# Kernel tuning notes

Measured on AMD Instinct MI355X. Metric: run time of the kernel, lower is better.

Reference implementation:

```python
import jax, jax.numpy as jnp
import numpy as np

B, T, E, H = 4, 1024, 1024, 16
D = E // H  # head_dim = 64


def setup_inputs() -> dict:
    key = jax.random.key(0)
    ks = jax.random.split(key, 6)
    s = 0.02  # realistic init scale for stable softmax
    return {
        "hidden_states": jax.random.normal(ks[0], (B, T, E), jnp.float32),
        "attention_mask": jnp.zeros((B, 1, T, T), jnp.float32),
        "Wq": jax.random.normal(ks[1], (E, E), jnp.float32) * s,
        "bq": jnp.zeros((E,), jnp.float32),
        "Wk": jax.random.normal(ks[2], (E, E), jnp.float32) * s,
        "bk": jnp.zeros((E,), jnp.float32),
        "Wv": jax.random.normal(ks[3], (E, E), jnp.float32) * s,
        "bv": jnp.zeros((E,), jnp.float32),
        "Wo": jax.random.normal(ks[4], (E, E), jnp.float32) * s,
        "bo": jnp.zeros((E,), jnp.float32),
    }


def reference(hidden_states, attention_mask, Wq, bq, Wk, bk, Wv, bv, Wo, bo):
    b, t, e = hidden_states.shape
    scaling = jnp.asarray(D, hidden_states.dtype) ** -0.5
    # q_proj weights/bias are pre-scaled in the module; equivalent to scaling q output
    q = (hidden_states @ Wq.T + bq) * scaling      # [B,T,E]
    k = hidden_states @ Wk.T + bk                   # self-attention path (no cache)
    v = hidden_states @ Wv.T + bv
    q = q.reshape(b, t, H, D)
    k = k.reshape(b, t, H, D)
    v = v.reshape(b, t, H, D)
    # bmm(q, k^T): [B,H,T,S] score matrix (materialized, as in the original)
    scores = jnp.einsum("bthd,bshd->bhts", q, k) + attention_mask
    probs = jax.nn.softmax(scores, axis=-1)
    ctx = jnp.einsum("bhts,bshd->bthd", probs, v).reshape(b, t, e)
    return ctx @ Wo.T + bo
```

## Files before the change

kernel.cpp:

```cpp
#include <hip/hip_runtime.h>
#include <math.h>

#define BB 4
#define TT 1024
#define EE 1024
#define HH 16
#define DD 64
#define KDIM 1024
#define N_HS (4096 * 1024)
#define N_W  (1024 * 1024)
#define NQKV (BB * HH * TT * DD)

typedef _Float16 f16x8 __attribute__((ext_vector_type(8)));
typedef float    f32x4 __attribute__((ext_vector_type(4)));

__device__ __forceinline__ unsigned short f2h(float x) {
    _Float16 h = (_Float16)x;
    return __builtin_bit_cast(unsigned short, h);
}
__device__ __forceinline__ void split_h(float x, unsigned short& hi, unsigned short& lo) {
    _Float16 h = (_Float16)x;
    hi = __builtin_bit_cast(unsigned short, h);
    lo = f2h(x - (float)h);
}

__device__ __forceinline__ void gload16(const void* g, void* l) {
    __builtin_amdgcn_global_load_lds(
        (const __attribute__((address_space(1))) void*)g,
        (__attribute__((address_space(3))) void*)l, 16, 0, 0);
}

__global__ __launch_bounds__(256)
void split_kernel(const float* __restrict__ hs,
                  const float* __restrict__ Wq, const float* __restrict__ Wk,
                  const float* __restrict__ Wv, const float* __restrict__ Wo,
                  unsigned short* __restrict__ ws)
{
    const int u = blockIdx.x * 256 + threadIdx.x;
    const float* src;
    unsigned short* dst;
    if (u < (N_HS / 4)) {
        src = hs + (size_t)u * 4;
        dst = ws + (size_t)u * 4;
    } else {
        int v = u - N_HS / 4;
        int wsel = v >> 18;
        int wo   = v & 0x3FFFF;
        const float* Wsrc = (wsel == 0) ? Wq : (wsel == 1) ? Wk : (wsel == 2) ? Wv : Wo;
        src = Wsrc + (size_t)wo * 4;
        dst = ws + (size_t)N_HS + (size_t)wsel * N_W + (size_t)wo * 4;
    }
    float4 x = *(const float4*)src;
    ushort4 h4;
    h4.x = f2h(x.x); h4.y = f2h(x.y); h4.z = f2h(x.z); h4.w = f2h(x.w);
    *(ushort4*)dst = h4;
}

__global__ __launch_bounds__(256)
void qkv_kernel(const unsigned short* __restrict__ hsp,
                const unsigned short* __restrict__ wqp,
                const float* __restrict__ bq, const float* __restrict__ bk,
                const float* __restrict__ bv,
                unsigned short* __restrict__ qkvb)
{
    __shared__ unsigned short Ah[128 * 32], Bh[128 * 32];

    const int widx  = blockIdx.x >> 3;
    const int nbase = (blockIdx.x & 7) * 128;
    const int mbase = blockIdx.y * 128;
    const unsigned short* Wp = wqp + (size_t)widx * N_W;
    const float* bias = (widx == 0) ? bq : (widx == 1) ? bk : bv;
    unsigned short* dst = qkvb + (size_t)widx * NQKV;
    const float scale = (widx == 0) ? 0.125f : 1.0f;

    const int tid  = threadIdx.x;
    const int w    = tid >> 6;
    const int lane = tid & 63;
    const int quad = lane >> 4;
    const int l16  = lane & 15;
    const int wm   = (w >> 1) * 64;
    const int wn   = (w & 1) * 64;

    f32x4 acc[4][4];
#pragma unroll
    for (int i = 0; i < 4; i++)
#pragma unroll
        for (int j = 0; j < 4; j++) acc[i][j] = (f32x4)0.f;

#pragma unroll 1
    for (int kt = 0; kt < KDIM; kt += 32) {
        __syncthreads();
#pragma unroll
        for (int i = 0; i < 2; i++) {
            int u = tid + i * 256;
            int r = u >> 2, c = u & 3;
            int q = c ^ ((r >> 1) & 3);
            gload16(hsp + (size_t)(mbase + r) * KDIM + kt + q * 8, &Ah[u * 8]);
            gload16(Wp  + (size_t)(nbase + r) * KDIM + kt + q * 8, &Bh[u * 8]);
        }
        __syncthreads();

        f16x8 af[4], bfr[4];
#pragma unroll
        for (int i = 0; i < 4; i++) {
            int r = wm + i * 16 + l16;
            af[i] = *(const f16x8*)&Ah[(r * 4 + (quad ^ ((r >> 1) & 3))) * 8];
        }
#pragma unroll
        for (int j = 0; j < 4; j++) {
            int r = wn + j * 16 + l16;
            bfr[j] = *(const f16x8*)&Bh[(r * 4 + (quad ^ ((r >> 1) & 3))) * 8];
        }
#pragma unroll
        for (int i = 0; i < 4; i++)
#pragma unroll
            for (int j = 0; j < 4; j++)
                acc[i][j] = __builtin_amdgcn_mfma_f32_16x16x32_f16(af[i], bfr[j], acc[i][j], 0, 0, 0);
    }

#pragma unroll
    for (int j = 0; j < 4; j++) {
        int n = nbase + wn + j * 16 + l16;
        int h = n >> 6, d = n & 63;
        float bj = bias[n];
#pragma unroll
        for (int i = 0; i < 4; i++)
#pragma unroll
            for (int rr = 0; rr < 4; rr++) {
                int m = mbase + wm + i * 16 + quad * 4 + rr;
                int b = m >> 10, t = m & 1023;
                dst[(((size_t)(b * HH + h) * TT + t) * DD + d)] =
                    f2h((acc[i][j][rr] + bj) * scale);
            }
    }
}

__global__ __launch_bounds__(256)
void outproj_kernel(const unsigned short* __restrict__ ctxh,
                    const unsigned short* __restrict__ ctxl,
                    const unsigned short* __restrict__ wop,
                    const float* __restrict__ bo, float* __restrict__ out)
{
    __shared__ unsigned short Ach[64 * 32], Acl[64 * 32], Bh[128 * 32];

    const int nbase = blockIdx.x * 128;
    const int mbase = blockIdx.y * 64;

    const int tid  = threadIdx.x;
    const int w    = tid >> 6;
    const int lane = tid & 63;
    const int quad = lane >> 4;
    const int l16  = lane & 15;
    const int wm   = (w >> 1) * 32;
    const int wn   = (w & 1) * 64;

    f32x4 acc[2][4];
#pragma unroll
    for (int i = 0; i < 2; i++)
#pragma unroll
        for (int j = 0; j < 4; j++) acc[i][j] = (f32x4)0.f;

#pragma unroll 1
    for (int kt = 0; kt < KDIM; kt += 32) {
        __syncthreads();
        {
            int r = tid >> 2, c = tid & 3;
            int q = c ^ ((r >> 1) & 3);
            size_t ga = (size_t)(mbase + r) * KDIM + kt + q * 8;
            gload16(ctxh + ga, &Ach[tid * 8]);
            gload16(ctxl + ga, &Acl[tid * 8]);
        }
#pragma unroll
        for (int i = 0; i < 2; i++) {
            int u = tid + i * 256;
            int r = u >> 2, c = u & 3;
            int q = c ^ ((r >> 1) & 3);
            gload16(wop + (size_t)(nbase + r) * KDIM + kt + q * 8, &Bh[u * 8]);
        }
        __syncthreads();

        f16x8 ah[2], al[2], bfr[4];
#pragma unroll
        for (int i = 0; i < 2; i++) {
            int r = wm + i * 16 + l16;
            int slot = (r * 4 + (quad ^ ((r >> 1) & 3))) * 8;
            ah[i] = *(const f16x8*)&Ach[slot];
            al[i] = *(const f16x8*)&Acl[slot];
        }
#pragma unroll
        for (int j = 0; j < 4; j++) {
            int r = wn + j * 16 + l16;
            bfr[j] = *(const f16x8*)&Bh[(r * 4 + (quad ^ ((r >> 1) & 3))) * 8];
        }
#pragma unroll
        for (int i = 0; i < 2; i++)
#pragma unroll
            for (int j = 0; j < 4; j++) {
                acc[i][j] = __builtin_amdgcn_mfma_f32_16x16x32_f16(ah[i], bfr[j], acc[i][j], 0, 0, 0);
                acc[i][j] = __builtin_amdgcn_mfma_f32_16x16x32_f16(al[i], bfr[j], acc[i][j], 0, 0, 0);
            }
    }

#pragma unroll
    for (int j = 0; j < 4; j++) {
        int n = nbase + wn + j * 16 + l16;
        float bj = bo[n];
#pragma unroll
        for (int i = 0; i < 2; i++)
#pragma unroll
            for (int rr = 0; rr < 4; rr++) {
                int m = mbase + wm + i * 16 + quad * 4 + rr;
                out[(size_t)m * EE + n] = acc[i][j][rr] + bj;
            }
    }
}

#define LS 72

__global__ __launch_bounds__(256)
void attn_kernel(const unsigned short* __restrict__ qp_, const unsigned short* __restrict__ kp_,
                 const unsigned short* __restrict__ vp_,
                 const float* __restrict__ mask,
                 unsigned short* __restrict__ ctxh, unsigned short* __restrict__ ctxl)
{
    __shared__ unsigned short Ks[64 * 64];
    __shared__ unsigned short Vt[64 * LS];
    __shared__ unsigned short Ps[64 * LS];

    const int bh = blockIdx.y;
    const int b  = bh >> 4;
    const int h  = bh & 15;
    const int m0 = blockIdx.x * 64;
    const size_t hoff = (size_t)bh * TT * DD;
    const unsigned short* qhp = qp_ + hoff;
    const unsigned short* khp = kp_ + hoff;
    const unsigned short* vhp = vp_ + hoff;
    const float* mb = mask + (size_t)b * TT * TT;

    const int tid  = threadIdx.x;
    const int w    = tid >> 6;
    const int lane = tid & 63;
    const int quad = lane >> 4;
    const int l16  = lane & 15;

    f16x8 qf[2];
#pragma unroll
    for (int s = 0; s < 2; s++)
        qf[s] = *(const f16x8*)(qhp + (size_t)(m0 + w * 16 + l16) * DD + s * 32 + quad * 8);

    f32x4 o[4];
    float m_i[4], l_i[4];
#pragma unroll
    for (int t = 0; t < 4; t++) o[t] = (f32x4)0.f;
#pragma unroll
    for (int r = 0; r < 4; r++) { m_i[r] = -INFINITY; l_i[r] = 0.f; }

    for (int n0 = 0; n0 < TT; n0 += 64) {
        float mreg[4][4];
#pragma unroll
        for (int t = 0; t < 4; t++)
#pragma unroll
            for (int r = 0; r < 4; r++)
                mreg[t][r] = mb[(size_t)(m0 + w * 16 + quad * 4 + r) * TT + n0 + 16 * t + l16];

        __syncthreads();
#pragma unroll
        for (int i = 0; i < 2; i++) {
            int u = tid + i * 256;
            int r = u >> 3, cp = u & 7;
            int c = cp ^ (r & 7);
            gload16(khp + (size_t)(n0 + r) * DD + c * 8, &Ks[u * 8]);
        }
        {
            int n  = tid & 63;
            int d0 = (tid >> 6) * 8;
#pragma unroll
            for (int half = 0; half < 2; half++) {
                int dd = d0 + half * 32;
                uint4 rv = *(const uint4*)(vhp + (size_t)(n0 + n) * DD + dd);
                unsigned int uu[4] = {rv.x, rv.y, rv.z, rv.w};
#pragma unroll
                for (int j = 0; j < 4; j++) {
                    Vt[(dd + 2 * j + 0) * LS + n] = (unsigned short)(uu[j] & 0xFFFFu);
                    Vt[(dd + 2 * j + 1) * LS + n] = (unsigned short)(uu[j] >> 16);
                }
            }
        }
        __syncthreads();

        f32x4 st[4];
#pragma unroll
        for (int t = 0; t < 4; t++) {
            f32x4 sv;
            sv[0] = mreg[t][0]; sv[1] = mreg[t][1]; sv[2] = mreg[t][2]; sv[3] = mreg[t][3];
            st[t] = sv;
        }
#pragma unroll
        for (int s = 0; s < 2; s++)
#pragma unroll
            for (int t = 0; t < 4; t++) {
                int R = 16 * t + l16;
                const f16x8 kf = *(const f16x8*)&Ks[(R * 8 + ((s * 4 + quad) ^ (R & 7))) * 8];
                st[t] = __builtin_amdgcn_mfma_f32_16x16x32_f16(qf[s], kf, st[t], 0, 0, 0);
            }

        float rm[4], rs[4], alpha[4];
#pragma unroll
        for (int r = 0; r < 4; r++)
            rm[r] = fmaxf(fmaxf(st[0][r], st[1][r]), fmaxf(st[2][r], st[3][r]));
#pragma unroll
        for (int mky = 1; mky < 16; mky <<= 1)
#pragma unroll
            for (int r = 0; r < 4; r++)
                rm[r] = fmaxf(rm[r], __shfl_xor(rm[r], mky));
#pragma unroll
        for (int r = 0; r < 4; r++) {
            float mn = fmaxf(m_i[r], rm[r]);
            alpha[r] = __expf(m_i[r] - mn);
            m_i[r]   = mn;
            rs[r]    = 0.f;
        }
#pragma unroll
        for (int t = 0; t < 4; t++)
#pragma unroll
            for (int r = 0; r < 4; r++) {
                float p = __expf(st[t][r] - m_i[r]);
                st[t][r] = p;
                rs[r] += p;
            }
#pragma unroll
        for (int mky = 1; mky < 16; mky <<= 1)
#pragma unroll
            for (int r = 0; r < 4; r++)
                rs[r] += __shfl_xor(rs[r], mky);
#pragma unroll
        for (int r = 0; r < 4; r++)
            l_i[r] = l_i[r] * alpha[r] + rs[r];
#pragma unroll
        for (int t = 0; t < 4; t++)
#pragma unroll
            for (int r = 0; r < 4; r++)
                o[t][r] *= alpha[r];

#pragma unroll
        for (int t = 0; t < 4; t++)
#pragma unroll
            for (int r = 0; r < 4; r++)
                Ps[(w * 16 + quad * 4 + r) * LS + 16 * t + l16] = f2h(st[t][r]);

#pragma unroll
        for (int s = 0; s < 2; s++) {
            const f16x8 pf = *(const f16x8*)&Ps[(w * 16 + l16) * LS + s * 32 + quad * 8];
#pragma unroll
            for (int t = 0; t < 4; t++) {
                const f16x8 vf = *(const f16x8*)&Vt[(16 * t + l16) * LS + s * 32 + quad * 8];
                o[t] = __builtin_amdgcn_mfma_f32_16x16x32_f16(pf, vf, o[t], 0, 0, 0);
            }
        }
    }

#pragma unroll
    for (int r = 0; r < 4; r++) {
        float inv = 1.0f / l_i[r];
        int m = m0 + w * 16 + quad * 4 + r;
#pragma unroll
        for (int t = 0; t < 4; t++) {
            float val = o[t][r] * inv;
            unsigned short hi, lo;
            split_h(val, hi, lo);
            size_t off = (size_t)(b * TT + m) * EE + h * DD + 16 * t + l16;
            ctxh[off] = hi;
            ctxl[off] = lo;
        }
    }
}

extern "C" void kernel_launch(void* const* d_in, const int* in_sizes, int n_in,
                              void* d_out, int out_size, void* d_ws, size_t ws_size,
                              hipStream_t stream)
{
    const float* hs   = (const float*)d_in[0];
    const float* mask = (const float*)d_in[1];
    const float* Wq   = (const float*)d_in[2];
    const float* bq   = (const float*)d_in[3];
    const float* Wk   = (const float*)d_in[4];
    const float* bk   = (const float*)d_in[5];
    const float* Wv   = (const float*)d_in[6];
    const float* bv   = (const float*)d_in[7];
    const float* Wo   = (const float*)d_in[8];
    const float* bo   = (const float*)d_in[9];
    float* out = (float*)d_out;

    unsigned short* ws   = (unsigned short*)d_ws;
    unsigned short* hsp  = ws;
    unsigned short* wqp  = ws + (size_t)N_HS;
    unsigned short* wop  = wqp + 3 * (size_t)N_W;
    unsigned short* qkvb = wqp + 4 * (size_t)N_W;
    unsigned short* qp   = qkvb;
    unsigned short* kp   = qp + (size_t)NQKV;
    unsigned short* vp   = kp + (size_t)NQKV;
    unsigned short* ctxh = ws;
    unsigned short* ctxl = qkvb + 3 * (size_t)NQKV;

    split_kernel<<<8192, 256, 0, stream>>>(hs, Wq, Wk, Wv, Wo, ws);
    qkv_kernel<<<dim3(24, 32), 256, 0, stream>>>(hsp, wqp, bq, bk, bv, qkvb);
    attn_kernel<<<dim3(TT / 64, BB * HH), 256, 0, stream>>>(qp, kp, vp, mask, ctxh, ctxl);
    outproj_kernel<<<dim3(8, 64), 256, 0, stream>>>(ctxh, ctxl, wop, bo, out);
}
```

Measured before the change: 230.6 us.

## Pre-transpose V in a separate kernel and async-load it into swizzled LDS

```diff
diff --git a/kernel.cpp b/kernel.cpp
--- a/kernel.cpp
+++ b/kernel.cpp
@@ -136,6 +136,40 @@
 }
 
 __global__ __launch_bounds__(256)
+void vtrans_kernel(const unsigned short* __restrict__ vp,
+                   unsigned short* __restrict__ vtp)
+{
+    __shared__ unsigned short Ts[64 * 72];
+    const int bh = blockIdx.y;
+    const int t0 = blockIdx.x * 64;
+    const unsigned short* src = vp  + (size_t)bh * TT * DD + (size_t)t0 * DD;
+    unsigned short*       dst = vtp + (size_t)bh * DD * TT + t0;
+    const int tid = threadIdx.x;
+
+#pragma unroll
+    for (int i = 0; i < 2; i++) {
+        int id = tid + i * 256;
+        int r = id >> 3, c = id & 7;
+        *(uint4*)&Ts[r * 72 + c * 8] = *(const uint4*)(src + (size_t)r * DD + c * 8);
+    }
+    __syncthreads();
+#pragma unroll
+    for (int i = 0; i < 2; i++) {
+        int id = tid + i * 256;
+        int d = id >> 3, c = id & 7;
+        unsigned short tmp[8];
+#pragma unroll
+        for (int j = 0; j < 8; j++) tmp[j] = Ts[(c * 8 + j) * 72 + d];
+        uint4 o;
+        o.x = (unsigned int)tmp[0] | ((unsigned int)tmp[1] << 16);
+        o.y = (unsigned int)tmp[2] | ((unsigned int)tmp[3] << 16);
+        o.z = (unsigned int)tmp[4] | ((unsigned int)tmp[5] << 16);
+        o.w = (unsigned int)tmp[6] | ((unsigned int)tmp[7] << 16);
+        *(uint4*)(dst + (size_t)d * TT + c * 8) = o;
+    }
+}
+
+__global__ __launch_bounds__(256)
 void outproj_kernel(const unsigned short* __restrict__ ctxh,
                     const unsigned short* __restrict__ ctxl,
                     const unsigned short* __restrict__ wop,
@@ -219,12 +253,12 @@
 
 __global__ __launch_bounds__(256)
 void attn_kernel(const unsigned short* __restrict__ qp_, const unsigned short* __restrict__ kp_,
-                 const unsigned short* __restrict__ vp_,
+                 const unsigned short* __restrict__ vtp_,
                  const float* __restrict__ mask,
                  unsigned short* __restrict__ ctxh, unsigned short* __restrict__ ctxl)
 {
     __shared__ unsigned short Ks[64 * 64];
-    __shared__ unsigned short Vt[64 * LS];
+    __shared__ unsigned short Vt[64 * 64];
     __shared__ unsigned short Ps[64 * LS];
 
     const int bh = blockIdx.y;
@@ -234,7 +268,7 @@
     const size_t hoff = (size_t)bh * TT * DD;
     const unsigned short* qhp = qp_ + hoff;
     const unsigned short* khp = kp_ + hoff;
-    const unsigned short* vhp = vp_ + hoff;
+    const unsigned short* vtp = vtp_ + hoff;
     const float* mb = mask + (size_t)b * TT * TT;
 
     const int tid  = threadIdx.x;
@@ -256,12 +290,12 @@
     for (int r = 0; r < 4; r++) { m_i[r] = -INFINITY; l_i[r] = 0.f; }
 
     for (int n0 = 0; n0 < TT; n0 += 64) {
-        float mreg[4][4];
+        f32x4 st[4];
 #pragma unroll
         for (int t = 0; t < 4; t++)
 #pragma unroll
             for (int r = 0; r < 4; r++)
-                mreg[t][r] = mb[(size_t)(m0 + w * 16 + quad * 4 + r) * TT + n0 + 16 * t + l16];
+                st[t][r] = mb[(size_t)(m0 + w * 16 + quad * 4 + r) * TT + n0 + 16 * t + l16];
 
         __syncthreads();
 #pragma unroll
@@ -270,31 +304,10 @@
             int r = u >> 3, cp = u & 7;
             int c = cp ^ (r & 7);
             gload16(khp + (size_t)(n0 + r) * DD + c * 8, &Ks[u * 8]);
-        }
-        {
-            int n  = tid & 63;
-            int d0 = (tid >> 6) * 8;
-#pragma unroll
-            for (int half = 0; half < 2; half++) {
-                int dd = d0 + half * 32;
-                uint4 rv = *(const uint4*)(vhp + (size_t)(n0 + n) * DD + dd);
-                unsigned int uu[4] = {rv.x, rv.y, rv.z, rv.w};
-#pragma unroll
-                for (int j = 0; j < 4; j++) {
-                    Vt[(dd + 2 * j + 0) * LS + n] = (unsigned short)(uu[j] & 0xFFFFu);
-                    Vt[(dd + 2 * j + 1) * LS + n] = (unsigned short)(uu[j] >> 16);
-                }
-            }
-        }
-        __syncthreads();
-
-        f32x4 st[4];
-#pragma unroll
-        for (int t = 0; t < 4; t++) {
-            f32x4 sv;
-            sv[0] = mreg[t][0]; sv[1] = mreg[t][1]; sv[2] = mreg[t][2]; sv[3] = mreg[t][3];
-            st[t] = sv;
-        }
+            gload16(vtp + (size_t)r * TT + n0 + c * 8,   &Vt[u * 8]);
+        }
+        __syncthreads();
+
 #pragma unroll
         for (int s = 0; s < 2; s++)
 #pragma unroll
@@ -353,7 +366,8 @@
             const f16x8 pf = *(const f16x8*)&Ps[(w * 16 + l16) * LS + s * 32 + quad * 8];
 #pragma unroll
             for (int t = 0; t < 4; t++) {
-                const f16x8 vf = *(const f16x8*)&Vt[(16 * t + l16) * LS + s * 32 + quad * 8];
+                int R = 16 * t + l16;
+                const f16x8 vf = *(const f16x8*)&Vt[(R * 8 + ((s * 4 + quad) ^ (R & 7))) * 8];
                 o[t] = __builtin_amdgcn_mfma_f32_16x16x32_f16(pf, vf, o[t], 0, 0, 0);
             }
         }
@@ -401,9 +415,11 @@
     unsigned short* vp   = kp + (size_t)NQKV;
     unsigned short* ctxh = ws;
     unsigned short* ctxl = qkvb + 3 * (size_t)NQKV;
+    unsigned short* vtp  = ctxl + (size_t)N_HS;
 
     split_kernel<<<8192, 256, 0, stream>>>(hs, Wq, Wk, Wv, Wo, ws);
     qkv_kernel<<<dim3(24, 32), 256, 0, stream>>>(hsp, wqp, bq, bk, bv, qkvb);
-    attn_kernel<<<dim3(TT / 64, BB * HH), 256, 0, stream>>>(qp, kp, vp, mask, ctxh, ctxl);
+    vtrans_kernel<<<dim3(TT / 64, BB * HH), 256, 0, stream>>>(vp, vtp);
+    attn_kernel<<<dim3(TT / 64, BB * HH), 256, 0, stream>>>(qp, kp, vtp, mask, ctxh, ctxl);
     outproj_kernel<<<dim3(8, 64), 256, 0, stream>>>(ctxh, ctxl, wop, bo, out);
 }
```

Result: no change. 228.8 us (-0.8%).

## Double-buffer K/V tiles, pre-transpose V in projection, and convert mask to fp16

Applied to the files above, without the earlier changes.

```diff
diff --git a/kernel.cpp b/kernel.cpp
--- a/kernel.cpp
+++ b/kernel.cpp
@@ -10,6 +10,7 @@
 #define N_HS (4096 * 1024)
 #define N_W  (1024 * 1024)
 #define NQKV (BB * HH * TT * DD)
+#define NMASK (BB * TT * TT)
 
 typedef _Float16 f16x8 __attribute__((ext_vector_type(8)));
 typedef float    f32x4 __attribute__((ext_vector_type(4)));
@@ -34,7 +35,9 @@
 void split_kernel(const float* __restrict__ hs,
                   const float* __restrict__ Wq, const float* __restrict__ Wk,
                   const float* __restrict__ Wv, const float* __restrict__ Wo,
-                  unsigned short* __restrict__ ws)
+                  const float* __restrict__ maskp,
+                  unsigned short* __restrict__ ws,
+                  unsigned short* __restrict__ maskh)
 {
     const int u = blockIdx.x * 256 + threadIdx.x;
     const float* src;
@@ -42,13 +45,17 @@
     if (u < (N_HS / 4)) {
         src = hs + (size_t)u * 4;
         dst = ws + (size_t)u * 4;
-    } else {
+    } else if (u < (N_HS / 4) + N_W) {
         int v = u - N_HS / 4;
         int wsel = v >> 18;
         int wo   = v & 0x3FFFF;
         const float* Wsrc = (wsel == 0) ? Wq : (wsel == 1) ? Wk : (wsel == 2) ? Wv : Wo;
         src = Wsrc + (size_t)wo * 4;
         dst = ws + (size_t)N_HS + (size_t)wsel * N_W + (size_t)wo * 4;
+    } else {
+        int v = u - (N_HS / 4) - N_W;
+        src = maskp + (size_t)v * 4;
+        dst = maskh + (size_t)v * 4;
     }
     float4 x = *(const float4*)src;
     ushort4 h4;
@@ -70,7 +77,6 @@
     const int mbase = blockIdx.y * 128;
     const unsigned short* Wp = wqp + (size_t)widx * N_W;
     const float* bias = (widx == 0) ? bq : (widx == 1) ? bk : bv;
-    unsigned short* dst = qkvb + (size_t)widx * NQKV;
     const float scale = (widx == 0) ? 0.125f : 1.0f;
 
     const int tid  = threadIdx.x;
@@ -118,20 +124,42 @@
                 acc[i][j] = __builtin_amdgcn_mfma_f32_16x16x32_f16(af[i], bfr[j], acc[i][j], 0, 0, 0);
     }
 
-#pragma unroll
-    for (int j = 0; j < 4; j++) {
-        int n = nbase + wn + j * 16 + l16;
-        int h = n >> 6, d = n & 63;
-        float bj = bias[n];
-#pragma unroll
-        for (int i = 0; i < 4; i++)
-#pragma unroll
-            for (int rr = 0; rr < 4; rr++) {
-                int m = mbase + wm + i * 16 + quad * 4 + rr;
-                int b = m >> 10, t = m & 1023;
-                dst[(((size_t)(b * HH + h) * TT + t) * DD + d)] =
-                    f2h((acc[i][j][rr] + bj) * scale);
-            }
+    if (widx == 2) {
+        unsigned short* vtp = qkvb + 2 * (size_t)NQKV;
+#pragma unroll
+        for (int j = 0; j < 4; j++) {
+            int n = nbase + wn + j * 16 + l16;
+            int h = n >> 6, d = n & 63;
+            float bj = bias[n];
+#pragma unroll
+            for (int i = 0; i < 4; i++) {
+                int m = mbase + wm + i * 16 + quad * 4;
+                int b = m >> 10, t0 = m & 1023;
+                ushort4 pk;
+                pk.x = f2h(acc[i][j][0] + bj);
+                pk.y = f2h(acc[i][j][1] + bj);
+                pk.z = f2h(acc[i][j][2] + bj);
+                pk.w = f2h(acc[i][j][3] + bj);
+                *(ushort4*)(vtp + ((size_t)(b * HH + h) * DD + d) * TT + t0) = pk;
+            }
+        }
+    } else {
+        unsigned short* dst = qkvb + (size_t)widx * NQKV;
+#pragma unroll
+        for (int j = 0; j < 4; j++) {
+            int n = nbase + wn + j * 16 + l16;
+            int h = n >> 6, d = n & 63;
+            float bj = bias[n];
+#pragma unroll
+            for (int i = 0; i < 4; i++)
+#pragma unroll
+                for (int rr = 0; rr < 4; rr++) {
+                    int m = mbase + wm + i * 16 + quad * 4 + rr;
+                    int b = m >> 10, t = m & 1023;
+                    dst[(((size_t)(b * HH + h) * TT + t) * DD + d)] =
+                        f2h((acc[i][j][rr] + bj) * scale);
+                }
+        }
     }
 }
 
@@ -215,17 +243,15 @@
     }
 }
 
-#define LS 72
-
 __global__ __launch_bounds__(256)
 void attn_kernel(const unsigned short* __restrict__ qp_, const unsigned short* __restrict__ kp_,
-                 const unsigned short* __restrict__ vp_,
-                 const float* __restrict__ mask,
+                 const unsigned short* __restrict__ vtp_,
+                 const unsigned short* __restrict__ maskh,
                  unsigned short* __restrict__ ctxh, unsigned short* __restrict__ ctxl)
 {
-    __shared__ unsigned short Ks[64 * 64];
-    __shared__ unsigned short Vt[64 * LS];
-    __shared__ unsigned short Ps[64 * LS];
+    __shared__ unsigned short Ks[2][64 * 64];
+    __shared__ unsigned short Vt[2][64 * 64];
+    __shared__ unsigned short Ps[64 * 64];
 
     const int bh = blockIdx.y;
     const int b  = bh >> 4;
@@ -234,8 +260,8 @@
     const size_t hoff = (size_t)bh * TT * DD;
     const unsigned short* qhp = qp_ + hoff;
     const unsigned short* khp = kp_ + hoff;
-    const unsigned short* vhp = vp_ + hoff;
-    const float* mb = mask + (size_t)b * TT * TT;
+    const unsigned short* vtp = vtp_ + hoff;
+    const _Float16* mb = (const _Float16*)(maskh + (size_t)b * TT * TT);
 
     const int tid  = threadIdx.x;
     const int w    = tid >> 6;
@@ -243,66 +269,62 @@
     const int quad = lane >> 4;
     const int l16  = lane & 15;
 
-    f16x8 qf[2];
-#pragma unroll
-    for (int s = 0; s < 2; s++)
-        qf[s] = *(const f16x8*)(qhp + (size_t)(m0 + w * 16 + l16) * DD + s * 32 + quad * 8);
-
-    f32x4 o[4];
-    float m_i[4], l_i[4];
-#pragma unroll
-    for (int t = 0; t < 4; t++) o[t] = (f32x4)0.f;
-#pragma unroll
-    for (int r = 0; r < 4; r++) { m_i[r] = -INFINITY; l_i[r] = 0.f; }
-
-    for (int n0 = 0; n0 < TT; n0 += 64) {
-        float mreg[4][4];
-#pragma unroll
-        for (int t = 0; t < 4; t++)
-#pragma unroll
-            for (int r = 0; r < 4; r++)
-                mreg[t][r] = mb[(size_t)(m0 + w * 16 + quad * 4 + r) * TT + n0 + 16 * t + l16];
-
-        __syncthreads();
+    auto stage = [&](int n0s, int bb) {
 #pragma unroll
         for (int i = 0; i < 2; i++) {
             int u = tid + i * 256;
             int r = u >> 3, cp = u & 7;
             int c = cp ^ (r & 7);
-            gload16(khp + (size_t)(n0 + r) * DD + c * 8, &Ks[u * 8]);
-        }
-        {
-            int n  = tid & 63;
-            int d0 = (tid >> 6) * 8;
-#pragma unroll
-            for (int half = 0; half < 2; half++) {
-                int dd = d0 + half * 32;
-                uint4 rv = *(const uint4*)(vhp + (size_t)(n0 + n) * DD + dd);
-                unsigned int uu[4] = {rv.x, rv.y, rv.z, rv.w};
-#pragma unroll
-                for (int j = 0; j < 4; j++) {
-                    Vt[(dd + 2 * j + 0) * LS + n] = (unsigned short)(uu[j] & 0xFFFFu);
-                    Vt[(dd + 2 * j + 1) * LS + n] = (unsigned short)(uu[j] >> 16);
-                }
-            }
-        }
+            gload16(khp + (size_t)(n0s + r) * DD + c * 8, &Ks[bb][u * 8]);
+            gload16(vtp + (size_t)r * TT + n0s + c * 8,   &Vt[bb][u * 8]);
+        }
+    };
+
+    f16x8 qf[2];
+#pragma unroll
+    for (int s = 0; s < 2; s++)
+        qf[s] = *(const f16x8*)(qhp + (size_t)(m0 + w * 16 + l16) * DD + s * 32 + quad * 8);
+
+    f32x4 o[4];
+    float m_i[4], l_i[4];
+#pragma unroll
+    for (int t = 0; t < 4; t++) o[t] = (f32x4)0.f;
+#pragma unroll
+    for (int r = 0; r < 4; r++) { m_i[r] = -INFINITY; l_i[r] = 0.f; }
+
+    stage(0, 0);
+
+#pragma unroll 1
+    for (int it = 0; it < TT / 64; it++) {
+        const int n0  = it * 64;
+        const int cur = it & 1;
+
         __syncthreads();
+        if (it + 1 < TT / 64) stage(n0 + 64, 1 - cur);
+
+        _Float16 mreg[4][4];
+#pragma unroll
+        for (int t = 0; t < 4; t++)
+#pragma unroll
+            for (int r = 0; r < 4; r++)
+                mreg[t][r] = mb[(size_t)(m0 + w * 16 + quad * 4 + r) * TT + n0 + 16 * t + l16];
 
         f32x4 st[4];
 #pragma unroll
-        for (int t = 0; t < 4; t++) {
-            f32x4 sv;
-            sv[0] = mreg[t][0]; sv[1] = mreg[t][1]; sv[2] = mreg[t][2]; sv[3] = mreg[t][3];
-            st[t] = sv;
-        }
+        for (int t = 0; t < 4; t++) st[t] = (f32x4)0.f;
 #pragma unroll
         for (int s = 0; s < 2; s++)
 #pragma unroll
             for (int t = 0; t < 4; t++) {
                 int R = 16 * t + l16;
-                const f16x8 kf = *(const f16x8*)&Ks[(R * 8 + ((s * 4 + quad) ^ (R & 7))) * 8];
+                const f16x8 kf = *(const f16x8*)&Ks[cur][(R * 8 + ((s * 4 + quad) ^ (R & 7))) * 8];
                 st[t] = __builtin_amdgcn_mfma_f32_16x16x32_f16(qf[s], kf, st[t], 0, 0, 0);
             }
+#pragma unroll
+        for (int t = 0; t < 4; t++)
+#pragma unroll
+            for (int r = 0; r < 4; r++)
+                st[t][r] += (float)mreg[t][r];
 
         float rm[4], rs[4], alpha[4];
 #pragma unroll
@@ -345,15 +367,20 @@
 #pragma unroll
         for (int t = 0; t < 4; t++)
 #pragma unroll
-            for (int r = 0; r < 4; r++)
-                Ps[(w * 16 + quad * 4 + r) * LS + 16 * t + l16] = f2h(st[t][r]);
+            for (int r = 0; r < 4; r++) {
+                int R = w * 16 + quad * 4 + r;
+                int j = 16 * t + l16;
+                Ps[R * 64 + (((j >> 3) ^ (R & 7)) * 8) + (j & 7)] = f2h(st[t][r]);
+            }
 
 #pragma unroll
         for (int s = 0; s < 2; s++) {
-            const f16x8 pf = *(const f16x8*)&Ps[(w * 16 + l16) * LS + s * 32 + quad * 8];
+            int Rr = w * 16 + l16;
+            const f16x8 pf = *(const f16x8*)&Ps[Rr * 64 + (((s * 4 + quad) ^ (Rr & 7)) * 8)];
 #pragma unroll
             for (int t = 0; t < 4; t++) {
-                const f16x8 vf = *(const f16x8*)&Vt[(16 * t + l16) * LS + s * 32 + quad * 8];
+                int R = 16 * t + l16;
+                const f16x8 vf = *(const f16x8*)&Vt[cur][(R * 8 + ((s * 4 + quad) ^ (R & 7))) * 8];
                 o[t] = __builtin_amdgcn_mfma_f32_16x16x32_f16(pf, vf, o[t], 0, 0, 0);
             }
         }
@@ -391,19 +418,20 @@
     const float* bo   = (const float*)d_in[9];
     float* out = (float*)d_out;
 
-    unsigned short* ws   = (unsigned short*)d_ws;
-    unsigned short* hsp  = ws;
-    unsigned short* wqp  = ws + (size_t)N_HS;
-    unsigned short* wop  = wqp + 3 * (size_t)N_W;
-    unsigned short* qkvb = wqp + 4 * (size_t)N_W;
-    unsigned short* qp   = qkvb;
-    unsigned short* kp   = qp + (size_t)NQKV;
-    unsigned short* vp   = kp + (size_t)NQKV;
-    unsigned short* ctxh = ws;
-    unsigned short* ctxl = qkvb + 3 * (size_t)NQKV;
-
-    split_kernel<<<8192, 256, 0, stream>>>(hs, Wq, Wk, Wv, Wo, ws);
+    unsigned short* ws    = (unsigned short*)d_ws;
+    unsigned short* hsp   = ws;
+    unsigned short* wqp   = ws + (size_t)N_HS;
+    unsigned short* wop   = wqp + 3 * (size_t)N_W;
+    unsigned short* qkvb  = wqp + 4 * (size_t)N_W;
+    unsigned short* qp    = qkvb;
+    unsigned short* kp    = qp + (size_t)NQKV;
+    unsigned short* vtp   = kp + (size_t)NQKV;
+    unsigned short* ctxl  = vtp + (size_t)NQKV;
+    unsigned short* maskh = ctxl + (size_t)N_HS;
+    unsigned short* ctxh  = ws;
+
+    split_kernel<<<12288, 256, 0, stream>>>(hs, Wq, Wk, Wv, Wo, mask, ws, maskh);
     qkv_kernel<<<dim3(24, 32), 256, 0, stream>>>(hsp, wqp, bq, bk, bv, qkvb);
-    attn_kernel<<<dim3(TT / 64, BB * HH), 256, 0, stream>>>(qp, kp, vp, mask, ctxh, ctxl);
+    attn_kernel<<<dim3(TT / 64, BB * HH), 256, 0, stream>>>(qp, kp, vtp, maskh, ctxh, ctxl);
     outproj_kernel<<<dim3(8, 64), 256, 0, stream>>>(ctxh, ctxl, wop, bo, out);
 }
```

Result: slower. 252.9 us (+9.7%).
